# Performance work log

Measured on AMD Instinct MI355X. Metric: run time of the kernel, lower is better.

## Reference

```python
import jax, jax.numpy as jnp
import numpy as np

N = 100000
D_IN = 512
D_OUT = 512
E = 3200000


def setup_inputs() -> dict:
    key = jax.random.key(0)
    ks = jax.random.split(key, 10)
    stdv = 1.0 / np.sqrt(D_OUT)
    return {
        "x": jax.random.normal(ks[0], (N, D_IN), dtype=jnp.float32),
        "w1": jax.random.uniform(ks[1], (D_IN, D_OUT), jnp.float32, -stdv, stdv),
        "w2": jax.random.uniform(ks[2], (D_IN, D_OUT), jnp.float32, -stdv, stdv),
        "w3": jax.random.uniform(ks[3], (D_IN, D_OUT), jnp.float32, -stdv, stdv),
        "b1": jax.random.uniform(ks[4], (D_OUT,), jnp.float32, -stdv, stdv),
        "b2": jax.random.uniform(ks[5], (D_OUT,), jnp.float32, -stdv, stdv),
        "b3": jax.random.uniform(ks[6], (D_OUT,), jnp.float32, -stdv, stdv),
        "edge_row": jax.random.randint(ks[7], (E,), 0, N, dtype=jnp.int32),
        "edge_col": jax.random.randint(ks[8], (E,), 0, N, dtype=jnp.int32),
        "edge_val": jax.random.uniform(ks[9], (E,), dtype=jnp.float32),
    }


def reference(x, w1, w2, w3, b1, b2, b3, edge_row, edge_col, edge_val):
    n = x.shape[0]
    # three dense projections
    support = x @ w1                      # [N, D_OUT]
    trans = x @ w2 + b2                   # [N, D_OUT]
    gate = jax.nn.sigmoid(x @ w3 + b3)    # [N, D_OUT]
    # sparse adj @ support as edge-list gather -> weighted -> segment_sum
    msgs = support[edge_col] * edge_val[:, None]            # [E, D_OUT]
    agg = jax.ops.segment_sum(msgs, edge_row, num_segments=n)
    out = jax.nn.relu(agg + b1)
    return trans + gate * (out - trans)
```

## Files before the change

### kernel.cpp

```cpp
#include <hip/hip_runtime.h>
#include <hip/hip_bf16.h>
#include <hip/hip_fp16.h>

#define D 512

typedef _Float16 half8 __attribute__((ext_vector_type(8)));
typedef _Float16 half4v __attribute__((ext_vector_type(4)));
typedef float floatx4 __attribute__((ext_vector_type(4)));


__global__ void k_f32_to_f16(const float* __restrict__ in, _Float16* __restrict__ out, int n4) {
  int i = blockIdx.x * blockDim.x + threadIdx.x;
  if (i >= n4) return;
  floatx4 v = __builtin_nontemporal_load((const floatx4*)in + i);
  half4v h;
  h[0] = (_Float16)v[0]; h[1] = (_Float16)v[1]; h[2] = (_Float16)v[2]; h[3] = (_Float16)v[3];
  ((half4v*)out)[i] = h;
}

__global__ void k_build_wt(const float* __restrict__ w1, const float* __restrict__ w2,
                           const float* __restrict__ w3, _Float16* __restrict__ wT) {
  int id = blockIdx.x * blockDim.x + threadIdx.x;
  if (id >= 3 * D * D) return;
  int jg = id >> 9;
  int k  = id & (D - 1);
  const float* w = (jg < D) ? w1 : (jg < 2 * D ? w2 : w3);
  int j = jg & (D - 1);
  wT[id] = (_Float16)w[k * D + j];
}


__global__ void k_count(const int* __restrict__ row, int* __restrict__ counts, int E) {
  int i = blockIdx.x * blockDim.x + threadIdx.x;
  if (i < E) atomicAdd(&counts[row[i]], 1);
}

__global__ __launch_bounds__(256) void k_scan1(const int* __restrict__ in, int* __restrict__ out,
                                               int* __restrict__ bsums, int n) {
  __shared__ int wsum[4];
  int t = threadIdx.x, lane = t & 63, wd = t >> 6;
  int i0 = blockIdx.x * 1024 + t * 4;
  int4 c = make_int4(0, 0, 0, 0);
  if (i0 + 3 < n) c = *(const int4*)(in + i0);
  else {
    if (i0 < n) c.x = in[i0];
    if (i0 + 1 < n) c.y = in[i0 + 1];
    if (i0 + 2 < n) c.z = in[i0 + 2];
  }
  int s1 = c.x, s2 = s1 + c.y, s3 = s2 + c.z, s4 = s3 + c.w;
  int x = s4;
#pragma unroll
  for (int o = 1; o < 64; o <<= 1) { int p = __shfl_up(x, o); if (lane >= o) x += p; }
  if (lane == 63) wsum[wd] = x;
  __syncthreads();
  int wex = 0;
  for (int k = 0; k < wd; ++k) wex += wsum[k];
  int base = wex + x - s4;
  if (i0 + 3 < n) *(int4*)(out + i0) = make_int4(base, base + s1, base + s2, base + s3);
  else {
    if (i0 < n) out[i0] = base;
    if (i0 + 1 < n) out[i0 + 1] = base + s1;
    if (i0 + 2 < n) out[i0 + 2] = base + s2;
  }
  if (t == 0) bsums[blockIdx.x] = wsum[0] + wsum[1] + wsum[2] + wsum[3];
}

__global__ void k_scan2(int* __restrict__ bsums, int* __restrict__ total_out, int nb) {
  __shared__ int w0;
  int t = threadIdx.x, lane = t & 63, wd = t >> 6;
  int v = (t < nb) ? bsums[t] : 0;
  int x = v;
#pragma unroll
  for (int o = 1; o < 64; o <<= 1) { int p = __shfl_up(x, o); if (lane >= o) x += p; }
  if (wd == 0 && lane == 63) w0 = x;
  __syncthreads();
  int excl = x - v + (wd ? w0 : 0);
  if (t < nb) bsums[t] = excl;
  if (t == 127) *total_out = w0 + x;
}

__global__ __launch_bounds__(256) void k_scan3(int* __restrict__ out, const int* __restrict__ bsums, int n) {
  int t = threadIdx.x;
  int i0 = blockIdx.x * 1024 + t * 4;
  int add = bsums[blockIdx.x];
  if (i0 + 3 < n) {
    int4 v = *(int4*)(out + i0);
    v.x += add; v.y += add; v.z += add; v.w += add;
    *(int4*)(out + i0) = v;
  } else {
    for (int k = 0; k < 4; ++k) if (i0 + k < n) out[i0 + k] += add;
  }
}

__global__ void k_scatter(const int* __restrict__ row, const int* __restrict__ col,
                          const float* __restrict__ val, const int* __restrict__ offsets,
                          int* __restrict__ cursor, long long* __restrict__ edges, int E) {
  int i = blockIdx.x * blockDim.x + threadIdx.x;
  if (i >= E) return;
  int r = row[i];
  int c = __builtin_nontemporal_load(col + i);
  float v = __builtin_nontemporal_load(val + i);
  int p = offsets[r] + atomicAdd(&cursor[r], 1);
  long long pack = ((long long)(unsigned)__float_as_int(v) << 32) | (unsigned)c;
  __builtin_nontemporal_store(pack, edges + p);
}

__global__ __launch_bounds__(256) void k_agg(
    const _Float16* __restrict__ xh, _Float16* __restrict__ yh,
    const int* __restrict__ offsets, const long long* __restrict__ edges, int n)
{
  int wid = (blockIdx.x * 256 + threadIdx.x) >> 6;
  if (wid >= n) return;
  int lane = threadIdx.x & 63;
  int s = offsets[wid], e = offsets[wid + 1];
  float acc[8] = {0, 0, 0, 0, 0, 0, 0, 0};
  const half8* x8 = (const half8*)xh;

  for (int base = s; base < e; base += 64) {
    int cnt = e - base; if (cnt > 64) cnt = 64;
    int key = 0x7fffffff; float val = 0.f;
    if (lane < cnt) {
      long long ed = __builtin_nontemporal_load(edges + base + lane);
      key = (int)(unsigned)(ed & 0xffffffffll);
      val = __int_as_float((int)(ed >> 32));
    }
#pragma unroll
    for (int size = 2; size <= 64; size <<= 1) {
#pragma unroll
      for (int stride = size >> 1; stride; stride >>= 1) {
        int pk = __shfl_xor(key, stride);
        float pv = __shfl_xor(val, stride);
        bool upper = (lane & stride) != 0;
        bool desc = (lane & size) != 0;
        bool takemax = upper != desc;
        bool swap = takemax ? (pk > key) : (pk < key);
        if (swap) { key = pk; val = pv; }
      }
    }
    int i = 0;
    for (; i + 8 <= cnt; i += 8) {
      int cc[8]; float vv[8];
#pragma unroll
      for (int u = 0; u < 8; ++u) { cc[u] = __shfl(key, i + u); vv[u] = __shfl(val, i + u); }
      half8 h[8];
#pragma unroll
      for (int u = 0; u < 8; ++u) h[u] = x8[(size_t)cc[u] * 64 + lane];
#pragma unroll
      for (int j = 0; j < 8; ++j) {
        float a = acc[j];
#pragma unroll
        for (int u = 0; u < 8; ++u) a += vv[u] * (float)h[u][j];
        acc[j] = a;
      }
    }
    for (; i + 4 <= cnt; i += 4) {
      int c0 = __shfl(key, i),     c1 = __shfl(key, i + 1);
      int c2 = __shfl(key, i + 2), c3 = __shfl(key, i + 3);
      float v0 = __shfl(val, i),     v1 = __shfl(val, i + 1);
      float v2 = __shfl(val, i + 2), v3 = __shfl(val, i + 3);
      half8 h0 = x8[(size_t)c0 * 64 + lane];
      half8 h1 = x8[(size_t)c1 * 64 + lane];
      half8 h2 = x8[(size_t)c2 * 64 + lane];
      half8 h3 = x8[(size_t)c3 * 64 + lane];
#pragma unroll
      for (int j = 0; j < 8; ++j)
        acc[j] += v0 * (float)h0[j] + v1 * (float)h1[j] + v2 * (float)h2[j] + v3 * (float)h3[j];
    }
    for (; i < cnt; ++i) {
      int c0 = __shfl(key, i);
      float v0 = __shfl(val, i);
      half8 h0 = x8[(size_t)c0 * 64 + lane];
#pragma unroll
      for (int j = 0; j < 8; ++j) acc[j] += v0 * (float)h0[j];
    }
  }

  half8 o;
#pragma unroll
  for (int j = 0; j < 8; ++j) o[j] = (_Float16)acc[j];
  ((half8*)yh)[(size_t)wid * 64 + lane] = o;
}

__global__ __launch_bounds__(256) void k_gemm_fused(
    const _Float16* __restrict__ Ax,
    const _Float16* __restrict__ Ay,
    const _Float16* __restrict__ BT,
    const float* __restrict__ b1, const float* __restrict__ b2,
    const float* __restrict__ b3, float* __restrict__ out, int M)
{
  __shared__ __align__(16) _Float16 ldsAx[128 * 32];
  __shared__ __align__(16) _Float16 ldsAy[128 * 32];
  __shared__ __align__(16) _Float16 ldsB[192 * 32];
  int t = threadIdx.x;
  int cb = blockIdx.x;
  int rowBase = blockIdx.y * 128;
  int w = t >> 6, lane = t & 63, lr = lane & 15, quad = lane >> 4;
  floatx4 acc[3][2][4] = {};

  int srow0 = lane >> 2;
  int schunk = lane & 3;

  for (int k0 = 0; k0 < D; k0 += 32) {
#pragma unroll
    for (int c = 0; c < 2; ++c) {
      int srow = w * 32 + c * 16 + srow0;
      int chunk = schunk ^ ((srow >> 1) & 3);
      int ga = rowBase + srow; if (ga >= M) ga = M - 1;
      const _Float16* gx = Ax + (size_t)ga * D + k0 + chunk * 8;
      const _Float16* gy = Ay + (size_t)ga * D + k0 + chunk * 8;
      _Float16* lx = &ldsAx[(w * 32 + c * 16) * 32];
      _Float16* ly = &ldsAy[(w * 32 + c * 16) * 32];
      __builtin_amdgcn_global_load_lds((const __attribute__((address_space(1))) void*)gx,
                                       (__attribute__((address_space(3))) void*)lx, 16, 0, 0);
      __builtin_amdgcn_global_load_lds((const __attribute__((address_space(1))) void*)gy,
                                       (__attribute__((address_space(3))) void*)ly, 16, 0, 0);
    }
#pragma unroll
    for (int c = 0; c < 3; ++c) {
      int srow = w * 48 + c * 16 + srow0;
      int chunk = schunk ^ ((srow >> 1) & 3);
      int m = srow >> 6, j = srow & 63;
      const _Float16* gB = BT + (size_t)(m * 512 + cb * 64 + j) * D + k0 + chunk * 8;
      _Float16* lB = &ldsB[(w * 48 + c * 16) * 32];
      __builtin_amdgcn_global_load_lds((const __attribute__((address_space(1))) void*)gB,
                                       (__attribute__((address_space(3))) void*)lB, 16, 0, 0);
    }
    __syncthreads();

    half8 afx[2], afy[2];
#pragma unroll
    for (int i2 = 0; i2 < 2; ++i2) {
      int r = w * 32 + i2 * 16 + lr;
      int sl = (quad ^ ((r >> 1) & 3)) << 3;
      afx[i2] = *(const half8*)&ldsAx[r * 32 + sl];
      afy[i2] = *(const half8*)&ldsAy[r * 32 + sl];
    }
#pragma unroll
    for (int m = 0; m < 3; ++m) {
      half8 bf[4];
#pragma unroll
      for (int f = 0; f < 4; ++f) {
        int r = m * 64 + f * 16 + lr;
        bf[f] = *(const half8*)&ldsB[r * 32 + ((quad ^ ((r >> 1) & 3)) << 3)];
      }
#pragma unroll
      for (int i2 = 0; i2 < 2; ++i2)
#pragma unroll
        for (int f = 0; f < 4; ++f)
          acc[m][i2][f] = __builtin_amdgcn_mfma_f32_16x16x32_f16(
              m == 0 ? afy[i2] : afx[i2], bf[f], acc[m][i2][f], 0, 0, 0);
    }
    __syncthreads();
  }

#pragma unroll
  for (int i2 = 0; i2 < 2; ++i2) {
    int r0 = rowBase + w * 32 + i2 * 16 + quad * 4;
#pragma unroll
    for (int f = 0; f < 4; ++f) {
      int c = cb * 64 + f * 16 + lr;
      float bb1 = b1[c], bb2 = b2[c], bb3 = b3[c];
#pragma unroll
      for (int rg = 0; rg < 4; ++rg) {
        int r = r0 + rg;
        if (r >= M) continue;
        float aggv = acc[0][i2][f][rg] + bb1;
        aggv = aggv > 0.f ? aggv : 0.f;
        float tr = acc[1][i2][f][rg] + bb2;
        float gv = acc[2][i2][f][rg] + bb3;
        gv = 1.0f / (1.0f + __expf(-gv));
        __builtin_nontemporal_store(tr + gv * (aggv - tr), &out[(size_t)r * D + c]);
      }
    }
  }
}


extern "C" void kernel_launch(void* const* d_in, const int* in_sizes, int n_in,
                              void* d_out, int out_size, void* d_ws, size_t ws_size,
                              hipStream_t stream) {
  const float* x    = (const float*)d_in[0];
  const float* w1   = (const float*)d_in[1];
  const float* w2   = (const float*)d_in[2];
  const float* w3   = (const float*)d_in[3];
  const float* b1   = (const float*)d_in[4];
  const float* b2   = (const float*)d_in[5];
  const float* b3   = (const float*)d_in[6];
  const int*   erow = (const int*)d_in[7];
  const int*   ecol = (const int*)d_in[8];
  const float* eval = (const float*)d_in[9];
  float* out = (float*)d_out;

  int N = in_sizes[0] / D;
  int E = in_sizes[7];

  char* ws = (char*)d_ws;
  size_t off = 0;
  auto take = [&](size_t bytes) -> char* {
    char* p = ws + off;
    off += (bytes + 255) & ~(size_t)255;
    return p;
  };
  _Float16* xh    = (_Float16*)take((size_t)N * D * 2);
  _Float16* yh    = (_Float16*)take((size_t)N * D * 2);
  _Float16* wT    = (_Float16*)take((size_t)3 * D * D * 2);
  int* counts     = (int*)take((size_t)N * 4);
  int* cursor     = (int*)take((size_t)N * 4);
  int* offsets    = (int*)take((size_t)(N + 1) * 4);
  int* bsums      = (int*)take(128 * 4);
  long long* edges = (long long*)take((size_t)E * 8);

  hipMemsetAsync(counts, 0, (size_t)N * 4, stream);
  hipMemsetAsync(cursor, 0, (size_t)N * 4, stream);

  int n4 = N * D / 4;
  k_f32_to_f16<<<(n4 + 255) / 256, 256, 0, stream>>>(x, xh, n4);
  k_build_wt<<<(3 * D * D + 255) / 256, 256, 0, stream>>>(w1, w2, w3, wT);
  k_count<<<(E + 255) / 256, 256, 0, stream>>>(erow, counts, E);
  int nb = (N + 1023) / 1024;
  k_scan1<<<nb, 256, 0, stream>>>(counts, offsets, bsums, N);
  k_scan2<<<1, 128, 0, stream>>>(bsums, offsets + N, nb);
  k_scan3<<<nb, 256, 0, stream>>>(offsets, bsums, N);
  k_scatter<<<(E + 255) / 256, 256, 0, stream>>>(erow, ecol, eval, offsets, cursor, edges, E);
  k_agg<<<((size_t)N * 64 + 255) / 256, 256, 0, stream>>>(xh, yh, offsets, edges, N);
  dim3 gg(D / 64, (N + 127) / 128);
  k_gemm_fused<<<gg, 256, 0, stream>>>(xh, yh, wT, b1, b2, b3, out, N);
}
```

Measured before the change: 1.369 ms.

## Double-buffer GEMM LDS, remap GEMM grid, split aggregation into half-row waves

The fused GEMM now double-buffers its LDS tiles so the next K-slice loads while MFMAs run on the current one, and a 1D grid is remapped to change block scheduling order. The aggregation kernel launches two waves per node, each handling half of the feature columns with 8-byte loads, to raise parallelism. The cost is doubled LDS use in the GEMM, which may cut occupancy, and the edge sort and shuffles are duplicated in aggregation.

```diff
diff --git a/kernel.cpp b/kernel.cpp
--- a/kernel.cpp
+++ b/kernel.cpp
@@ -109,12 +109,15 @@
     const _Float16* __restrict__ xh, _Float16* __restrict__ yh,
     const int* __restrict__ offsets, const long long* __restrict__ edges, int n)
 {
-  int wid = (blockIdx.x * 256 + threadIdx.x) >> 6;
-  if (wid >= n) return;
+  int gwid = (blockIdx.x * 256 + threadIdx.x) >> 6;
+  if (gwid >= 2 * n) return;
+  int half = (gwid >= n) ? 1 : 0;
+  int wid = half ? (gwid - n) : gwid;
   int lane = threadIdx.x & 63;
   int s = offsets[wid], e = offsets[wid + 1];
-  float acc[8] = {0, 0, 0, 0, 0, 0, 0, 0};
-  const half8* x8 = (const half8*)xh;
+  float acc[4] = {0, 0, 0, 0};
+  const half4v* x4 = (const half4v*)xh;
+  int cidx = half * 64 + lane;
 
   for (int base = s; base < e; base += 64) {
     int cnt = e - base; if (cnt > 64) cnt = 64;
@@ -142,11 +145,11 @@
       int cc[8]; float vv[8];
 #pragma unroll
       for (int u = 0; u < 8; ++u) { cc[u] = __shfl(key, i + u); vv[u] = __shfl(val, i + u); }
-      half8 h[8];
-#pragma unroll
-      for (int u = 0; u < 8; ++u) h[u] = x8[(size_t)cc[u] * 64 + lane];
-#pragma unroll
-      for (int j = 0; j < 8; ++j) {
+      half4v h[8];
+#pragma unroll
+      for (int u = 0; u < 8; ++u) h[u] = x4[(size_t)cc[u] * 128 + cidx];
+#pragma unroll
+      for (int j = 0; j < 4; ++j) {
         float a = acc[j];
 #pragma unroll
         for (int u = 0; u < 8; ++u) a += vv[u] * (float)h[u][j];
@@ -158,27 +161,27 @@
       int c2 = __shfl(key, i + 2), c3 = __shfl(key, i + 3);
       float v0 = __shfl(val, i),     v1 = __shfl(val, i + 1);
       float v2 = __shfl(val, i + 2), v3 = __shfl(val, i + 3);
-      half8 h0 = x8[(size_t)c0 * 64 + lane];
-      half8 h1 = x8[(size_t)c1 * 64 + lane];
-      half8 h2 = x8[(size_t)c2 * 64 + lane];
-      half8 h3 = x8[(size_t)c3 * 64 + lane];
-#pragma unroll
-      for (int j = 0; j < 8; ++j)
+      half4v h0 = x4[(size_t)c0 * 128 + cidx];
+      half4v h1 = x4[(size_t)c1 * 128 + cidx];
+      half4v h2 = x4[(size_t)c2 * 128 + cidx];
+      half4v h3 = x4[(size_t)c3 * 128 + cidx];
+#pragma unroll
+      for (int j = 0; j < 4; ++j)
         acc[j] += v0 * (float)h0[j] + v1 * (float)h1[j] + v2 * (float)h2[j] + v3 * (float)h3[j];
     }
     for (; i < cnt; ++i) {
       int c0 = __shfl(key, i);
       float v0 = __shfl(val, i);
-      half8 h0 = x8[(size_t)c0 * 64 + lane];
-#pragma unroll
-      for (int j = 0; j < 8; ++j) acc[j] += v0 * (float)h0[j];
-    }
-  }
-
-  half8 o;
-#pragma unroll
-  for (int j = 0; j < 8; ++j) o[j] = (_Float16)acc[j];
-  ((half8*)yh)[(size_t)wid * 64 + lane] = o;
+      half4v h0 = x4[(size_t)c0 * 128 + cidx];
+#pragma unroll
+      for (int j = 0; j < 4; ++j) acc[j] += v0 * (float)h0[j];
+    }
+  }
+
+  half4v o;
+#pragma unroll
+  for (int j = 0; j < 4; ++j) o[j] = (_Float16)acc[j];
+  ((half4v*)yh)[(size_t)wid * 128 + cidx] = o;
 }
 
 __global__ __launch_bounds__(256) void k_gemm_fused(
@@ -188,19 +191,22 @@
     const float* __restrict__ b1, const float* __restrict__ b2,
     const float* __restrict__ b3, float* __restrict__ out, int M)
 {
-  __shared__ __align__(16) _Float16 ldsAx[128 * 32];
-  __shared__ __align__(16) _Float16 ldsAy[128 * 32];
-  __shared__ __align__(16) _Float16 ldsB[192 * 32];
+  __shared__ __align__(16) _Float16 ldsAx[2][128 * 32];
+  __shared__ __align__(16) _Float16 ldsAy[2][128 * 32];
+  __shared__ __align__(16) _Float16 ldsB[2][192 * 32];
   int t = threadIdx.x;
-  int cb = blockIdx.x;
-  int rowBase = blockIdx.y * 128;
+  int nrb = (M + 127) >> 7;
+  int bid = blockIdx.x;
+  int wq = (bid & 7) * nrb + (bid >> 3);
+  int rowBase = (wq >> 3) << 7;
+  int cb = wq & 7;
   int w = t >> 6, lane = t & 63, lr = lane & 15, quad = lane >> 4;
   floatx4 acc[3][2][4] = {};
 
   int srow0 = lane >> 2;
   int schunk = lane & 3;
 
-  for (int k0 = 0; k0 < D; k0 += 32) {
+  auto stage = [&](int buf, int k0) {
 #pragma unroll
     for (int c = 0; c < 2; ++c) {
       int srow = w * 32 + c * 16 + srow0;
@@ -208,8 +214,8 @@
       int ga = rowBase + srow; if (ga >= M) ga = M - 1;
       const _Float16* gx = Ax + (size_t)ga * D + k0 + chunk * 8;
       const _Float16* gy = Ay + (size_t)ga * D + k0 + chunk * 8;
-      _Float16* lx = &ldsAx[(w * 32 + c * 16) * 32];
-      _Float16* ly = &ldsAy[(w * 32 + c * 16) * 32];
+      _Float16* lx = &ldsAx[buf][(w * 32 + c * 16) * 32];
+      _Float16* ly = &ldsAy[buf][(w * 32 + c * 16) * 32];
       __builtin_amdgcn_global_load_lds((const __attribute__((address_space(1))) void*)gx,
                                        (__attribute__((address_space(3))) void*)lx, 16, 0, 0);
       __builtin_amdgcn_global_load_lds((const __attribute__((address_space(1))) void*)gy,
@@ -221,19 +227,26 @@
       int chunk = schunk ^ ((srow >> 1) & 3);
       int m = srow >> 6, j = srow & 63;
       const _Float16* gB = BT + (size_t)(m * 512 + cb * 64 + j) * D + k0 + chunk * 8;
-      _Float16* lB = &ldsB[(w * 48 + c * 16) * 32];
+      _Float16* lB = &ldsB[buf][(w * 48 + c * 16) * 32];
       __builtin_amdgcn_global_load_lds((const __attribute__((address_space(1))) void*)gB,
                                        (__attribute__((address_space(3))) void*)lB, 16, 0, 0);
     }
-    __syncthreads();
+  };
+
+  stage(0, 0);
+  __syncthreads();
+
+  for (int kt = 0; kt < 16; ++kt) {
+    int cur = kt & 1;
+    if (kt < 15) stage(cur ^ 1, (kt + 1) * 32);
 
     half8 afx[2], afy[2];
 #pragma unroll
     for (int i2 = 0; i2 < 2; ++i2) {
       int r = w * 32 + i2 * 16 + lr;
       int sl = (quad ^ ((r >> 1) & 3)) << 3;
-      afx[i2] = *(const half8*)&ldsAx[r * 32 + sl];
-      afy[i2] = *(const half8*)&ldsAy[r * 32 + sl];
+      afx[i2] = *(const half8*)&ldsAx[cur][r * 32 + sl];
+      afy[i2] = *(const half8*)&ldsAy[cur][r * 32 + sl];
     }
 #pragma unroll
     for (int m = 0; m < 3; ++m) {
@@ -241,7 +254,7 @@
 #pragma unroll
       for (int f = 0; f < 4; ++f) {
         int r = m * 64 + f * 16 + lr;
-        bf[f] = *(const half8*)&ldsB[r * 32 + ((quad ^ ((r >> 1) & 3)) << 3)];
+        bf[f] = *(const half8*)&ldsB[cur][r * 32 + ((quad ^ ((r >> 1) & 3)) << 3)];
       }
 #pragma unroll
       for (int i2 = 0; i2 < 2; ++i2)
@@ -322,7 +335,7 @@
   k_scan2<<<1, 128, 0, stream>>>(bsums, offsets + N, nb);
   k_scan3<<<nb, 256, 0, stream>>>(offsets, bsums, N);
   k_scatter<<<(E + 255) / 256, 256, 0, stream>>>(erow, ecol, eval, offsets, cursor, edges, E);
-  k_agg<<<((size_t)N * 64 + 255) / 256, 256, 0, stream>>>(xh, yh, offsets, edges, N);
-  dim3 gg(D / 64, (N + 127) / 128);
-  k_gemm_fused<<<gg, 256, 0, stream>>>(xh, yh, wT, b1, b2, b3, out, N);
-}
+  k_agg<<<((size_t)2 * N * 64 + 255) / 256, 256, 0, stream>>>(xh, yh, offsets, edges, N);
+  int nrb = (N + 127) / 128;
+  k_gemm_fused<<<nrb * 8, 256, 0, stream>>>(xh, yh, wT, b1, b2, b3, out, N);
+}
```

Result: slower. 1.405 ms (+2.6%).
